# Performance work log

Hardware: AMD Instinct MI355X
Metric: run time of the kernel (lower is better)

Reference implementation:

```python
import jax, jax.numpy as jnp
import numpy as np

COMMITMENT_COST = 0.25


def setup_inputs() -> dict:
    key = jax.random.key(0)
    k1, k2 = jax.random.split(key)
    ze = jax.random.normal(k1, (16, 256, 32, 32), dtype=jnp.float32)
    codebook = jax.random.normal(k2, (8192, 256), dtype=jnp.float32) * 0.02
    return {"ze": ze, "codebook": codebook}


def reference(ze, codebook):
    # ze: [B, C, H, W] -> [B, H, W, C]
    B, C, H, W = ze.shape
    ze_nhwc = jnp.transpose(ze, (0, 2, 3, 1))
    ze_flat = ze_nhwc.reshape(B * H * W, C)

    # squared L2 distances to every codebook row: [B*H*W, vocab]
    distances = (
        jnp.sum(ze_flat ** 2, axis=1, keepdims=True)
        + jnp.sum(codebook ** 2, axis=1)
        - 2.0 * ze_flat @ codebook.T
    )
    encoding_indices = jnp.argmin(distances, axis=1)  # [B*H*W]
    zq = codebook[encoding_indices].reshape(B, H, W, C)

    sg = jax.lax.stop_gradient
    quantization_loss = jnp.mean((sg(ze_nhwc) - zq) ** 2)
    commitment_loss = jnp.mean((ze_nhwc - sg(zq)) ** 2)
    vq_loss = quantization_loss + COMMITMENT_COST * commitment_loss

    # straight-through estimator (training mode)
    zq = ze_nhwc + sg(zq - ze_nhwc)
    zq = jnp.transpose(zq, (0, 3, 1, 2))  # back to [B, C, H, W]
    return vq_loss, zq, encoding_indices.reshape(B, H * W)
```

## Files before the change

kernel.cpp:

```cpp
#include <hip/hip_runtime.h>
#include <hip/hip_bf16.h>

#define NPIX 16384
#define NVOC 8192
#define CHUNK 32

typedef short short8v __attribute__((ext_vector_type(8)));
typedef float floatx4 __attribute__((ext_vector_type(4)));

#define WS_ZEBF   0u
#define WS_BLIST  0u
#define WS_PART   0u
#define WS_CBBF   8388608u
#define WS_PK     8388608u
#define WS_TAU    8519680u
#define WS_ZEF    12582912u
#define WS_MIN    29360128u
#define WS_BN     37748736u
#define WS_AN     37781504u
#define WS_BCNT   37847040u
#define WS_BMAXU  37847552u
#define WS_QCNT   37847556u
#define WS_QUEUE  37847808u

__device__ __forceinline__ short f2bf(float v) {
  __bf16 h = (__bf16)v;
  return __builtin_bit_cast(short, h);
}

__device__ __forceinline__ unsigned long long packdj(float d, int j) {
  return ((unsigned long long)__float_as_uint(d) << 32) | (unsigned int)j;
}

__device__ __forceinline__ void gll16(const void* g, void* l) {
  __builtin_amdgcn_global_load_lds(
      (const __attribute__((address_space(1))) void*)g,
      (__attribute__((address_space(3))) void*)l, 16, 0, 0);
}

__device__ __forceinline__ float np_pairwise128_sq(const float* x, int stride) {
  float r[8];
#pragma unroll
  for (int j = 0; j < 8; ++j) {
    float v = x[j * stride];
    r[j] = __fmul_rn(v, v);
  }
#pragma unroll
  for (int i = 1; i < 16; ++i) {
#pragma unroll
    for (int j = 0; j < 8; ++j) {
      float v = x[(i * 8 + j) * stride];
      r[j] = __fadd_rn(r[j], __fmul_rn(v, v));
    }
  }
  return __fadd_rn(__fadd_rn(__fadd_rn(r[0], r[1]), __fadd_rn(r[2], r[3])),
                   __fadd_rn(__fadd_rn(r[4], r[5]), __fadd_rn(r[6], r[7])));
}

__global__ __launch_bounds__(256) void k_bnorm(const float* __restrict__ cb,
                                               float* __restrict__ bn,
                                               unsigned* __restrict__ bmaxu) {
  __shared__ float rows[64][257];
  int tid = threadIdx.x;
  int c0 = blockIdx.x * 64;
  for (int r = 0; r < 64; ++r)
    rows[r][tid] = cb[(size_t)(c0 + r) * 256 + tid];
  __syncthreads();
  if (tid < 64) {
    float a = np_pairwise128_sq(&rows[tid][0], 1);
    float b = np_pairwise128_sq(&rows[tid][128], 1);
    float v = __fadd_rn(a, b);
    bn[c0 + tid] = v;
    atomicMax(bmaxu, __float_as_uint(v));
  }
}

__global__ __launch_bounds__(256) void k_cvt_ze(const float* __restrict__ ze,
                                                short* __restrict__ zebff,
                                                float* __restrict__ zef,
                                                float* __restrict__ an) {
  __shared__ float t[64][132];
  int tid = threadIdx.x;
  int p0 = blockIdx.x * 64;
  int b = p0 >> 10, hw0 = p0 & 1023;
  const float* src = ze + (size_t)b * 262144 + hw0;
  float apart = 0.f;
  for (int half = 0; half < 2; ++half) {
    if (half) __syncthreads();
    {
      int hw = tid & 63, cq = tid >> 6;
#pragma unroll
      for (int i = 0; i < 32; ++i) {
        int cl = i * 4 + cq;
        t[hw][cl] = src[(size_t)(half * 128 + cl) * 1024 + hw];
      }
    }
    __syncthreads();
    {
      int r = tid >> 2, cg = tid & 3;
      float* fd = zef + (size_t)(p0 + r) * 256 + half * 128 + cg * 32;
#pragma unroll
      for (int s = 0; s < 8; ++s) {
        float4 v = *reinterpret_cast<const float4*>(&t[r][cg * 32 + s * 4]);
        *reinterpret_cast<float4*>(fd + s * 4) = v;
      }
    }
    {
      int pg_l = tid >> 6, l = tid & 63;
      size_t pg = (size_t)(p0 >> 4) + pg_l;
      int lr = l & 15, lg = l >> 4;
#pragma unroll
      for (int kl = 0; kl < 4; ++kl) {
        int ks = half * 4 + kl;
        short8v v8;
#pragma unroll
        for (int e = 0; e < 8; ++e)
          v8[e] = f2bf(t[pg_l * 16 + lr][kl * 32 + lg * 8 + e]);
        *reinterpret_cast<short8v*>(zebff + (pg * 8 + ks) * 512 + l * 8) = v8;
      }
    }
    if (tid < 64) {
      float a = np_pairwise128_sq(&t[tid][0], 1);
      apart = half ? __fadd_rn(apart, a) : a;
    }
  }
  if (tid < 64) an[p0 + tid] = apart;
}

__global__ __launch_bounds__(256) void k_cvt_cb(const float* __restrict__ cb,
                                                short* __restrict__ cbbft,
                                                unsigned* __restrict__ bmaxu,
                                                int* __restrict__ qcnt) {
  __shared__ short t[64][264];
  int tid = threadIdx.x;
  if (blockIdx.x == 0 && tid == 0) {
    bmaxu[0] = 0u;
    qcnt[0] = 0;
  }
  int j0 = blockIdx.x * 64;
  {
    int col = tid >> 2, q = tid & 3;
    const float* src = cb + (size_t)(j0 + col) * 256 + q * 64;
#pragma unroll
    for (int i = 0; i < 8; ++i) {
      float4 a = *reinterpret_cast<const float4*>(src + i * 8);
      float4 b = *reinterpret_cast<const float4*>(src + i * 8 + 4);
      short8v v;
      v[0] = f2bf(a.x); v[1] = f2bf(a.y); v[2] = f2bf(a.z); v[3] = f2bf(a.w);
      v[4] = f2bf(b.x); v[5] = f2bf(b.y); v[6] = f2bf(b.z); v[7] = f2bf(b.w);
      *reinterpret_cast<short8v*>(&t[col][q * 64 + i * 8]) = v;
    }
  }
  __syncthreads();
  short* dst = cbbft + (size_t)blockIdx.x * 16384;
#pragma unroll
  for (int s = 0; s < 8; ++s) {
    int cid = tid + s * 256;
    int kc = cid >> 6, c2 = cid & 63;
    short8v v = *reinterpret_cast<const short8v*>(&t[c2][kc * 8]);
    *reinterpret_cast<short8v*>(dst + cid * 8) = v;
  }
}

__global__ __launch_bounds__(256, 2) void k_gemm(const short* __restrict__ zebff,
                                                 const short* __restrict__ cbbft,
                                                 const float* __restrict__ bn,
                                                 float* __restrict__ wsmin) {
  __shared__ short lds[32768];
  __shared__ float bnlds[1024];
  int tid = threadIdx.x;
  int lane = tid & 63, w = tid >> 6;
  int g = lane >> 4, r16 = lane & 15;
  int oct = blockIdx.x & 7, chunk = blockIdx.x >> 3;
  int p0 = chunk * 256;
  int ncol0 = oct * 1024;

  short8v pix[4][8];
  {
    const short* base = zebff + ((size_t)(p0 >> 4) + w * 4) * 4096 + lane * 8;
#pragma unroll
    for (int pf = 0; pf < 4; ++pf)
#pragma unroll
      for (int ks = 0; ks < 8; ++ks)
        pix[pf][ks] =
            *reinterpret_cast<const short8v*>(base + pf * 4096 + ks * 512);
  }
  gll16(bn + ncol0 + tid * 4, &bnlds[tid * 4]);

#define STAGE(t, boff)                                                         \
  {                                                                            \
    const short* src_ = cbbft + (size_t)(oct * 16 + (t)) * 16384;              \
    _Pragma("unroll") for (int s = 0; s < 8; ++s) {                            \
      int cid_ = tid + s * 256;                                                \
      gll16(src_ + cid_ * 8, &lds[(boff) + cid_ * 8]);                         \
    }                                                                          \
  }
  STAGE(0, 0)
  asm volatile("s_waitcnt vmcnt(0)" ::: "memory");
  __builtin_amdgcn_s_barrier();

  float* wbase = wsmin + (size_t)(oct * 16) * NPIX + p0 + w * 64 + r16;

  for (int t = 0; t < 16; ++t) {
    int bA = (t & 1) * 16384;
    int bC = bA ^ 16384;
    if (t < 15) STAGE(t + 1, bC)
    float4 bnv[4];
#pragma unroll
    for (int cf = 0; cf < 4; ++cf)
      bnv[cf] =
          *reinterpret_cast<const float4*>(&bnlds[t * 64 + cf * 16 + g * 4]);
    floatx4 acc[4][4];
#pragma unroll
    for (int cf = 0; cf < 4; ++cf)
#pragma unroll
      for (int pf = 0; pf < 4; ++pf) acc[cf][pf] = floatx4{0.f, 0.f, 0.f, 0.f};
    __builtin_amdgcn_s_setprio(1);
#pragma unroll
    for (int ks = 0; ks < 8; ++ks) {
      short8v cfr[4];
#pragma unroll
      for (int cf = 0; cf < 4; ++cf)
        cfr[cf] = *reinterpret_cast<const short8v*>(
            &lds[bA + (((ks * 4 + g) * 64) + cf * 16 + r16) * 8]);
#pragma unroll
      for (int cf = 0; cf < 4; ++cf)
#pragma unroll
        for (int pf = 0; pf < 4; ++pf)
          acc[cf][pf] = __builtin_amdgcn_mfma_f32_16x16x32_bf16(
              cfr[cf], pix[pf][ks], acc[cf][pf], 0, 0, 0);
    }
    __builtin_amdgcn_s_setprio(0);
    float pmin[4];
#pragma unroll
    for (int pf = 0; pf < 4; ++pf) {
      float m_ = 3.4e38f;
#pragma unroll
      for (int cf = 0; cf < 4; ++cf)
#pragma unroll
        for (int rr = 0; rr < 4; ++rr)
          m_ = fminf(m_, __builtin_fmaf(-2.0f, acc[cf][pf][rr], bnv[cf][rr]));
      m_ = fminf(m_, __shfl_xor(m_, 16));
      m_ = fminf(m_, __shfl_xor(m_, 32));
      pmin[pf] = m_;
    }
    if (lane < 16) {
#pragma unroll
      for (int pf = 0; pf < 4; ++pf)
        wbase[(size_t)t * NPIX + pf * 16] = pmin[pf];
    }
    if (t < 15) asm volatile("s_waitcnt vmcnt(4)" ::: "memory");
    __builtin_amdgcn_s_barrier();
  }
#undef STAGE
}

__global__ __launch_bounds__(256) void k_tau(const float* __restrict__ wsmin,
                                             const float* __restrict__ an,
                                             const unsigned* __restrict__ bmaxu,
                                             float* __restrict__ tau,
                                             unsigned long long* __restrict__ pk) {
  __shared__ float sm[4][64];
  int tid = threadIdx.x;
  int px = tid & 63, q = tid >> 6;
  int p = blockIdx.x * 64 + px;
  float m0 = 3.4e38f, m1 = 3.4e38f, m2 = 3.4e38f, m3 = 3.4e38f;
#pragma unroll
  for (int i = 0; i < 8; ++i) {
    int c = q * 32 + i * 4;
    m0 = fminf(m0, wsmin[(size_t)c * NPIX + p]);
    m1 = fminf(m1, wsmin[(size_t)(c + 1) * NPIX + p]);
    m2 = fminf(m2, wsmin[(size_t)(c + 2) * NPIX + p]);
    m3 = fminf(m3, wsmin[(size_t)(c + 3) * NPIX + p]);
  }
  sm[q][px] = fminf(fminf(m0, m1), fminf(m2, m3));
  __syncthreads();
  if (tid < 64) {
    float m = fminf(fminf(sm[0][tid], sm[1][tid]), fminf(sm[2][tid], sm[3][tid]));
    float bmaxf = sqrtf(__uint_as_float(bmaxu[0]));
    tau[p] = m + 0.017f * sqrtf(an[p]) * bmaxf + 2e-4f;
    pk[p] = ~0ull;
  }
}

__global__ __launch_bounds__(256) void k_compact(const float* __restrict__ wsmin,
                                                 const float* __restrict__ tau,
                                                 const float* __restrict__ cb,
                                                 float* __restrict__ cbsw,
                                                 int* __restrict__ bcnt,
                                                 int* __restrict__ blist,
                                                 int* __restrict__ qcnt,
                                                 int* __restrict__ queue) {
  __shared__ int wbase[4];
  __shared__ int running;
  int c = blockIdx.x;
  const float* row = wsmin + (size_t)c * NPIX;
  int* dst = blist + (size_t)c * NPIX;
  int tid = threadIdx.x;
  int lane = tid & 63, wv = tid >> 6;
  if (tid == 0) running = 0;
  __syncthreads();
  for (int base = 0; base < NPIX; base += 256) {
    int p = base + tid;
    bool flag = row[p] <= tau[p];
    unsigned long long mask = __ballot(flag);
    int cnt = __popcll(mask);
    int pre = __popcll(mask & ((1ull << lane) - 1ull));
    if (lane == 0) wbase[wv] = cnt;
    __syncthreads();
    if (tid == 0) {
      int r = running;
#pragma unroll
      for (int w2 = 0; w2 < 4; ++w2) {
        int t = wbase[w2];
        wbase[w2] = r;
        r += t;
      }
      running = r;
    }
    __syncthreads();
    if (flag) dst[wbase[wv] + pre] = p;
    __syncthreads();
  }
  if (tid == 0) {
    int n = running;
    bcnt[c] = n;
    int nch = (n + CHUNK - 1) / CHUNK;
    if (nch > 0) {
      int q0 = atomicAdd(qcnt, nch * 2);
      for (int i = 0; i < nch; ++i) {
        queue[q0 + 2 * i] = (2 * c) | (i << 16);
        queue[q0 + 2 * i + 1] = (2 * c + 1) | (i << 16);
      }
    }
  }
  {
    const float4* cb4 = reinterpret_cast<const float4*>(cb);
    float4* dst4 = reinterpret_cast<float4*>(cbsw);
#pragma unroll
    for (int i = 0; i < 16; ++i) {
      int gid = tid + i * 256;
      int jj = 64 * c + (gid >> 6), u = gid & 63;
      dst4[(size_t)jj * 64 + u] = cb4[(size_t)jj * 64 + (u ^ (jj & 7))];
    }
  }
}

__global__ __launch_bounds__(256, 2) void k_rescore_b(
    const float* __restrict__ zef, const float* __restrict__ cbsw,
    const float* __restrict__ an, const float* __restrict__ bn,
    const int* __restrict__ bcnt, const int* __restrict__ blist,
    const int* __restrict__ qcnt, const int* __restrict__ queue,
    unsigned long long* __restrict__ pk) {
  __shared__ float zl[32 * 256];
  __shared__ float cstf[32 * 256];
  __shared__ int pidx[32];
  __shared__ float apx[32];
  int tid = threadIdx.x;
  int lane = tid & 63, wv = tid >> 6;
  int code32 = lane & 31, half = lane >> 5;
  int nq = qcnt[0];
  for (int qi = blockIdx.x; qi < nq; qi += 512) {
    int e = queue[qi];
    int g = e & 0xffff, chunk = e >> 16;
    int c = g >> 1;
    int n = bcnt[c];
    int base = chunk * CHUNK;
    int cnt_here = min(CHUNK, n - base);
    __syncthreads();
#pragma unroll
    for (int i = 0; i < 8; ++i) {
      int px = wv * 8 + i;
      int idx = base + min(px, cnt_here - 1);
      int p = blist[(size_t)c * NPIX + idx];
      gll16(zef + (size_t)p * 256 + lane * 4, &zl[px * 256 + lane * 4]);
    }
#pragma unroll
    for (int i = 0; i < 8; ++i) {
      int r = wv * 8 + i;
      gll16(cbsw + (size_t)(g * 32 + r) * 256 + lane * 4,
            &cstf[r * 256 + lane * 4]);
    }
    if (tid < 32) {
      int idx = base + min(tid, cnt_here - 1);
      int p = blist[(size_t)c * NPIX + idx];
      pidx[tid] = p;
      apx[tid] = an[p];
    }
    asm volatile("s_waitcnt vmcnt(0)" ::: "memory");
    __syncthreads();
    int jg = g * 32 + code32;
    float bnj = bn[jg];
    int px0 = wv * 8 + half * 4;
    int sw = code32 & 7;
    const float* crow = &cstf[code32 * 256];
    float acc[4] = {0.f, 0.f, 0.f, 0.f};
#pragma unroll 8
    for (int k4 = 0; k4 < 64; ++k4) {
      float4 cv = *reinterpret_cast<const float4*>(&crow[(k4 ^ sw) << 2]);
#pragma unroll
      for (int i = 0; i < 4; ++i) {
        float4 zv =
            *reinterpret_cast<const float4*>(&zl[(px0 + i) * 256 + k4 * 4]);
        acc[i] = __builtin_fmaf(zv.x, cv.x, acc[i]);
        acc[i] = __builtin_fmaf(zv.y, cv.y, acc[i]);
        acc[i] = __builtin_fmaf(zv.z, cv.z, acc[i]);
        acc[i] = __builtin_fmaf(zv.w, cv.w, acc[i]);
      }
    }
#pragma unroll
    for (int i = 0; i < 4; ++i) {
      int px = px0 + i;
      float d = __fsub_rn(__fadd_rn(apx[px], bnj), 2.0f * acc[i]);
      unsigned long long q = packdj(d, jg);
#pragma unroll
      for (int off = 1; off < 32; off <<= 1) {
        unsigned long long q2 = __shfl_xor(q, off);
        q = q2 < q ? q2 : q;
      }
      if (code32 == 0) atomicMin(&pk[pidx[px]], q);
    }
  }
}

__global__ __launch_bounds__(256) void k_gather(const float* __restrict__ ze,
                                                const float* __restrict__ cb,
                                                const unsigned long long* __restrict__ pk,
                                                float* __restrict__ out_zq,
                                                float* __restrict__ out_idx,
                                                float* __restrict__ part) {
  __shared__ float qrow[64][257];
  __shared__ int sidx[64];
  int tid = threadIdx.x;
  int p0 = blockIdx.x * 64;
  int b = p0 >> 10, hw0 = p0 & 1023;
  if (tid < 64) {
    int bi = (int)(unsigned int)(pk[p0 + tid] & 0xffffffffull);
    sidx[tid] = bi;
    out_idx[p0 + tid] = (float)bi;
  }
  __syncthreads();
  for (int r = 0; r < 64; ++r)
    qrow[r][tid] = cb[(size_t)sidx[r] * 256 + tid];
  __syncthreads();
  float lsum = 0.f;
  size_t zbase = (size_t)b * 262144 + hw0;
#pragma unroll 4
  for (int i = 0; i < 64; ++i) {
    int px = tid & 63;
    int c = i * 4 + (tid >> 6);
    float qv = qrow[px][c];
    size_t gi = zbase + (size_t)c * 1024 + px;
    float zev = ze[gi];
    out_zq[gi] = __fadd_rn(zev, __fsub_rn(qv, zev));
    float d = zev - qv;
    lsum = __builtin_fmaf(d, d, lsum);
  }
#pragma unroll
  for (int off = 32; off; off >>= 1) lsum += __shfl_xor(lsum, off, 64);
  __shared__ float wsum[4];
  if ((tid & 63) == 0) wsum[tid >> 6] = lsum;
  __syncthreads();
  if (tid == 0) part[blockIdx.x] = (wsum[0] + wsum[1]) + (wsum[2] + wsum[3]);
}

__global__ __launch_bounds__(256) void k_final(const float* __restrict__ part,
                                               float* __restrict__ out0) {
  int tid = threadIdx.x;
  float s = part[tid];
#pragma unroll
  for (int off = 32; off; off >>= 1) s += __shfl_xor(s, off, 64);
  __shared__ float wsum[4];
  if ((tid & 63) == 0) wsum[tid >> 6] = s;
  __syncthreads();
  if (tid == 0)
    out0[0] = 1.25f * ((wsum[0] + wsum[1]) + (wsum[2] + wsum[3])) / 4194304.0f;
}

extern "C" void kernel_launch(void* const* d_in, const int* in_sizes, int n_in,
                              void* d_out, int out_size, void* d_ws, size_t ws_size,
                              hipStream_t stream) {
  const float* ze = (const float*)d_in[0];
  const float* cb = (const float*)d_in[1];
  float* out = (float*)d_out;
  char* ws = (char*)d_ws;
  short* zebff = (short*)(ws + WS_ZEBF);
  short* cbbft = (short*)(ws + WS_CBBF);
  float* zef = (float*)(ws + WS_ZEF);
  float* bn = (float*)(ws + WS_BN);
  float* an = (float*)(ws + WS_AN);
  float* wsmin = (float*)(ws + WS_MIN);
  float* cbsw = (float*)(ws + WS_MIN);
  float* tau = (float*)(ws + WS_TAU);
  int* blist = (int*)(ws + WS_BLIST);
  int* bcnt = (int*)(ws + WS_BCNT);
  unsigned* bmaxu = (unsigned*)(ws + WS_BMAXU);
  int* qcnt = (int*)(ws + WS_QCNT);
  int* queue = (int*)(ws + WS_QUEUE);
  unsigned long long* pk = (unsigned long long*)(ws + WS_PK);
  float* part = (float*)(ws + WS_PART);
  float* out_loss = out;
  float* out_zq = out + 1;
  float* out_idx = out + 1 + 4194304;

  k_cvt_ze<<<256, 256, 0, stream>>>(ze, zebff, zef, an);
  k_cvt_cb<<<128, 256, 0, stream>>>(cb, cbbft, bmaxu, qcnt);
  k_bnorm<<<128, 256, 0, stream>>>(cb, bn, bmaxu);
  k_gemm<<<512, 256, 0, stream>>>(zebff, cbbft, bn, wsmin);
  k_tau<<<256, 256, 0, stream>>>(wsmin, an, bmaxu, tau, pk);
  k_compact<<<128, 256, 0, stream>>>(wsmin, tau, cb, cbsw, bcnt, blist, qcnt,
                                     queue);
  k_rescore_b<<<512, 256, 0, stream>>>(zef, cbsw, an, bn, bcnt, blist, qcnt,
                                       queue, pk);
  k_gather<<<256, 256, 0, stream>>>(ze, cb, pk, out_zq, out_idx, part);
  k_final<<<1, 256, 0, stream>>>(part, out_loss);
}
```

Measured before the change: 174.0 us.

## Load codebook MFMA fragments directly from global memory instead of LDS staging

The codebook bf16 conversion now writes data in an MFMA-fragment-ready layout, so each lane can load its operand with one contiguous 16-byte global load. The GEMM kernel drops the double-buffered LDS staging, the barriers and the LDS copy of the codebook norms, and reads the fragments and norms straight from global memory (L2-cached) with the loop unrolled by two. This removes LDS traffic and barrier synchronisation. In exchange every wave fetches the codebook tile itself, so global and L2 traffic rises and load latency is no longer hidden by an explicit prefetch.

```diff
diff --git a/kernel.cpp b/kernel.cpp
--- a/kernel.cpp
+++ b/kernel.cpp
@@ -128,7 +128,7 @@
 }
 
 __global__ __launch_bounds__(256) void k_cvt_cb(const float* __restrict__ cb,
-                                                short* __restrict__ cbbft,
+                                                short* __restrict__ cbff,
                                                 unsigned* __restrict__ bmaxu,
                                                 int* __restrict__ qcnt) {
   __shared__ short t[64][264];
@@ -152,22 +152,23 @@
     }
   }
   __syncthreads();
-  short* dst = cbbft + (size_t)blockIdx.x * 16384;
+  short* dst = cbff + (size_t)blockIdx.x * 16384;
 #pragma unroll
   for (int s = 0; s < 8; ++s) {
-    int cid = tid + s * 256;
-    int kc = cid >> 6, c2 = cid & 63;
-    short8v v = *reinterpret_cast<const short8v*>(&t[c2][kc * 8]);
-    *reinterpret_cast<short8v*>(dst + cid * 8) = v;
+    int id = tid + s * 256;
+    int rec = id >> 6, l = id & 63;
+    int cf = rec & 3, ks = rec >> 2;
+    int code = cf * 16 + (l & 15);
+    int k = ks * 32 + (l >> 4) * 8;
+    short8v v = *reinterpret_cast<const short8v*>(&t[code][k]);
+    *reinterpret_cast<short8v*>(dst + id * 8) = v;
   }
 }
 
 __global__ __launch_bounds__(256, 2) void k_gemm(const short* __restrict__ zebff,
-                                                 const short* __restrict__ cbbft,
+                                                 const short* __restrict__ cbff,
                                                  const float* __restrict__ bn,
                                                  float* __restrict__ wsmin) {
-  __shared__ short lds[32768];
-  __shared__ float bnlds[1024];
   int tid = threadIdx.x;
   int lane = tid & 63, w = tid >> 6;
   int g = lane >> 4, r16 = lane & 15;
@@ -185,31 +186,17 @@
         pix[pf][ks] =
             *reinterpret_cast<const short8v*>(base + pf * 4096 + ks * 512);
   }
-  gll16(bn + ncol0 + tid * 4, &bnlds[tid * 4]);
-
-#define STAGE(t, boff)                                                         \
-  {                                                                            \
-    const short* src_ = cbbft + (size_t)(oct * 16 + (t)) * 16384;              \
-    _Pragma("unroll") for (int s = 0; s < 8; ++s) {                            \
-      int cid_ = tid + s * 256;                                                \
-      gll16(src_ + cid_ * 8, &lds[(boff) + cid_ * 8]);                         \
-    }                                                                          \
-  }
-  STAGE(0, 0)
-  asm volatile("s_waitcnt vmcnt(0)" ::: "memory");
-  __builtin_amdgcn_s_barrier();
-
+  const short* cbase = cbff + (size_t)(oct * 16) * 16384;
   float* wbase = wsmin + (size_t)(oct * 16) * NPIX + p0 + w * 64 + r16;
 
+#pragma unroll 2
   for (int t = 0; t < 16; ++t) {
-    int bA = (t & 1) * 16384;
-    int bC = bA ^ 16384;
-    if (t < 15) STAGE(t + 1, bC)
+    const short* tb = cbase + t * 16384;
     float4 bnv[4];
 #pragma unroll
     for (int cf = 0; cf < 4; ++cf)
-      bnv[cf] =
-          *reinterpret_cast<const float4*>(&bnlds[t * 64 + cf * 16 + g * 4]);
+      bnv[cf] = *reinterpret_cast<const float4*>(
+          &bn[ncol0 + t * 64 + cf * 16 + g * 4]);
     floatx4 acc[4][4];
 #pragma unroll
     for (int cf = 0; cf < 4; ++cf)
@@ -222,7 +209,7 @@
 #pragma unroll
       for (int cf = 0; cf < 4; ++cf)
         cfr[cf] = *reinterpret_cast<const short8v*>(
-            &lds[bA + (((ks * 4 + g) * 64) + cf * 16 + r16) * 8]);
+            tb + (ks * 4 + cf) * 512 + lane * 8);
 #pragma unroll
       for (int cf = 0; cf < 4; ++cf)
 #pragma unroll
@@ -236,10 +223,12 @@
     for (int pf = 0; pf < 4; ++pf) {
       float m_ = 3.4e38f;
 #pragma unroll
-      for (int cf = 0; cf < 4; ++cf)
-#pragma unroll
-        for (int rr = 0; rr < 4; ++rr)
-          m_ = fminf(m_, __builtin_fmaf(-2.0f, acc[cf][pf][rr], bnv[cf][rr]));
+      for (int cf = 0; cf < 4; ++cf) {
+        m_ = fminf(m_, __builtin_fmaf(-2.0f, acc[cf][pf][0], bnv[cf].x));
+        m_ = fminf(m_, __builtin_fmaf(-2.0f, acc[cf][pf][1], bnv[cf].y));
+        m_ = fminf(m_, __builtin_fmaf(-2.0f, acc[cf][pf][2], bnv[cf].z));
+        m_ = fminf(m_, __builtin_fmaf(-2.0f, acc[cf][pf][3], bnv[cf].w));
+      }
       m_ = fminf(m_, __shfl_xor(m_, 16));
       m_ = fminf(m_, __shfl_xor(m_, 32));
       pmin[pf] = m_;
@@ -249,10 +238,7 @@
       for (int pf = 0; pf < 4; ++pf)
         wbase[(size_t)t * NPIX + pf * 16] = pmin[pf];
     }
-    if (t < 15) asm volatile("s_waitcnt vmcnt(4)" ::: "memory");
-    __builtin_amdgcn_s_barrier();
-  }
-#undef STAGE
+  }
 }
 
 __global__ __launch_bounds__(256) void k_tau(const float* __restrict__ wsmin,
@@ -485,7 +471,7 @@
   float* out = (float*)d_out;
   char* ws = (char*)d_ws;
   short* zebff = (short*)(ws + WS_ZEBF);
-  short* cbbft = (short*)(ws + WS_CBBF);
+  short* cbff = (short*)(ws + WS_CBBF);
   float* zef = (float*)(ws + WS_ZEF);
   float* bn = (float*)(ws + WS_BN);
   float* an = (float*)(ws + WS_AN);
@@ -504,9 +490,9 @@
   float* out_idx = out + 1 + 4194304;
 
   k_cvt_ze<<<256, 256, 0, stream>>>(ze, zebff, zef, an);
-  k_cvt_cb<<<128, 256, 0, stream>>>(cb, cbbft, bmaxu, qcnt);
+  k_cvt_cb<<<128, 256, 0, stream>>>(cb, cbff, bmaxu, qcnt);
   k_bnorm<<<128, 256, 0, stream>>>(cb, bn, bmaxu);
-  k_gemm<<<512, 256, 0, stream>>>(zebff, cbbft, bn, wsmin);
+  k_gemm<<<512, 256, 0, stream>>>(zebff, cbff, bn, wsmin);
   k_tau<<<256, 256, 0, stream>>>(wsmin, an, bmaxu, tau, pk);
   k_compact<<<128, 256, 0, stream>>>(wsmin, tau, cb, cbsw, bcnt, blist, qcnt,
                                      queue);
```

After: 199.7 us. +14.7%, slower.
